# Kernel optimization log

Hardware: AMD Instinct MI355X
Metric: run time of the kernel (lower is better)

Reference implementation:

```python
import jax, jax.numpy as jnp
import numpy as np

VOCAB = 50000
EMB = 256
HID = 256
MAX_PRED = 30
B = 64
S_ENC = 100


def setup_inputs() -> dict:
    key = jax.random.key(0)
    ks = jax.random.split(key, 16)
    s = 1.0 / np.sqrt(HID)
    return {
        "comment": jax.random.randint(ks[0], (B, 29), 0, VOCAB),
        "comment_input": jax.random.randint(ks[1], (B, 30), 0, VOCAB),
        "tok_output": jax.random.normal(ks[2], (B, S_ENC, HID), jnp.float32),
        "tok_enc_hc": jax.random.normal(ks[3], (1, B, HID), jnp.float32),
        "sbtao_output": jax.random.normal(ks[4], (B, S_ENC, HID), jnp.float32),
        "wemb": jax.random.normal(ks[5], (VOCAB, EMB), jnp.float32) * 0.02,
        "W_ih": jax.random.uniform(ks[6], (3 * HID, EMB), jnp.float32, -s, s),
        "W_hh": jax.random.uniform(ks[7], (3 * HID, HID), jnp.float32, -s, s),
        "b_ih": jax.random.uniform(ks[8], (3 * HID,), jnp.float32, -s, s),
        "b_hh": jax.random.uniform(ks[9], (3 * HID,), jnp.float32, -s, s),
        "W1": jax.random.uniform(ks[10], (HID, 3 * HID), jnp.float32, -s, s),
        "b1": jax.random.uniform(ks[11], (HID,), jnp.float32, -s, s),
        "W2": jax.random.uniform(ks[12], (VOCAB, HID), jnp.float32, -s, s),
        "b2": jax.random.uniform(ks[13], (VOCAB,), jnp.float32, -s, s),
    }


def _decode(comment_input, T, tok_output, h0, sbtao_output,
            wemb, W_ih, W_hh, b_ih, b_hh, W1, b1, W2, b2):
    # h0: [B,H]. The torch code re-uses hidden=tok_enc_hc at EVERY step,
    # so each step is an independent GRU-cell step -> vectorize over T.
    bsz = comment_input.shape[0]
    H = h0.shape[-1]
    emb = wemb[comment_input[:, :T]]                      # [B,T,E]
    gi = emb @ W_ih.T + b_ih                              # [B,T,3H]
    gh = h0 @ W_hh.T + b_hh                               # [B,3H]
    gh = gh[:, None, :]                                   # broadcast over T
    r = jax.nn.sigmoid(gi[..., :H] + gh[..., :H])
    z = jax.nn.sigmoid(gi[..., H:2 * H] + gh[..., H:2 * H])
    n = jnp.tanh(gi[..., 2 * H:] + r * gh[..., 2 * H:])
    dec = (1.0 - z) * n + z * h0[:, None, :]              # [B,T,H]

    def attend(enc):  # enc: [B,S,H]
        S = enc.shape[1]
        # Faithful to torch: keys come from a RESHAPE [B,S,H] -> [B,H,S]
        # (memory reinterpretation), not a transpose.
        keys = enc.reshape(bsz, H, S)
        a = jax.nn.softmax(jnp.einsum('bth,bhs->bts', dec, keys), axis=-1)
        return jnp.einsum('bts,bsh->bth', a, enc)         # [B,T,H]

    ctx = attend(tok_output)
    ast_ctx = attend(sbtao_output)
    cat = jnp.concatenate([ctx, dec, ast_ctx], axis=-1)   # [B,T,3H]
    out = jax.nn.relu(cat @ W1.T + b1)                    # [B,T,H]
    out = jax.nn.relu(out @ W2.T + b2)                    # [B,T,V]
    logprobs = jax.nn.log_softmax(out, axis=-1)           # [B,T,V]
    return logprobs


def reference(comment, comment_input, tok_output, tok_enc_hc, sbtao_output,
              wemb, W_ih, W_hh, b_ih, b_hh, W1, b1, W2, b2):
    T = min(comment.shape[1] + 1, MAX_PRED)
    h0 = tok_enc_hc[0]
    logprobs = _decode(comment_input, T, tok_output, h0, sbtao_output,
                       wemb, W_ih, W_hh, b_ih, b_hh, W1, b1, W2, b2)
    seq = jnp.argmax(logprobs, axis=-1).astype(jnp.int64 if jax.config.jax_enable_x64 else jnp.int32)
    return seq, logprobs
```

## Files before the change

kernel.cpp:

```cpp
#include <hip/hip_runtime.h>
#include <hip/hip_bf16.h>
#include <math.h>

#define NROW 1920
#define VOCAB_ 50000
#define NPAD 50048
#define NBLK 391
#define LDBF 72

typedef __attribute__((ext_vector_type(8))) short short8;
typedef __attribute__((ext_vector_type(4))) float floatx4;

__device__ inline ushort f32_to_bf16_bits(float f) {
    union { float f; unsigned u; } v; v.f = f;
    unsigned u = v.u;
    u += 0x7fffu + ((u >> 16) & 1u);
    return (ushort)(u >> 16);
}

__global__ void gather_emb_kernel(const int* __restrict__ tokens,
                                  const float* __restrict__ wemb,
                                  float* __restrict__ emb) {
    int n = blockIdx.x;
    int e = threadIdx.x;
    int tok = tokens[n];
    emb[(size_t)n * 256 + e] = wemb[(size_t)tok * 256 + e];
}

template <bool RELU>
__global__ __launch_bounds__(256) void gemm_nt_kernel(
    const float* __restrict__ A, const float* __restrict__ Bm,
    const float* __restrict__ bias, float* __restrict__ C,
    int M, int N, int K) {
    __shared__ float As[32][68];
    __shared__ float Bs[32][68];

    const int tid = threadIdx.x;
    const int m0 = blockIdx.y * 64;
    const int n0 = blockIdx.x * 64;
    const int tx = tid & 15;
    const int ty = tid >> 4;
    const int lrow = tid >> 3;
    const int lcol = (tid & 7) * 4;

    float acc[4][4];
#pragma unroll
    for (int i = 0; i < 4; ++i)
#pragma unroll
        for (int j = 0; j < 4; ++j) acc[i][j] = 0.f;

    for (int k0 = 0; k0 < K; k0 += 32) {
#pragma unroll
        for (int half = 0; half < 2; ++half) {
            int m = lrow + half * 32;
            float4 av = *reinterpret_cast<const float4*>(
                A + (size_t)(m0 + m) * K + k0 + lcol);
            As[lcol + 0][m] = av.x; As[lcol + 1][m] = av.y;
            As[lcol + 2][m] = av.z; As[lcol + 3][m] = av.w;
            int n = lrow + half * 32;
            float4 bv = make_float4(0.f, 0.f, 0.f, 0.f);
            if (n0 + n < N)
                bv = *reinterpret_cast<const float4*>(
                    Bm + (size_t)(n0 + n) * K + k0 + lcol);
            Bs[lcol + 0][n] = bv.x; Bs[lcol + 1][n] = bv.y;
            Bs[lcol + 2][n] = bv.z; Bs[lcol + 3][n] = bv.w;
        }
        __syncthreads();
#pragma unroll
        for (int k = 0; k < 32; ++k) {
            float4 a4 = *reinterpret_cast<const float4*>(&As[k][ty * 4]);
            float4 b4 = *reinterpret_cast<const float4*>(&Bs[k][tx * 4]);
            float a[4] = {a4.x, a4.y, a4.z, a4.w};
            float b[4] = {b4.x, b4.y, b4.z, b4.w};
#pragma unroll
            for (int i = 0; i < 4; ++i)
#pragma unroll
                for (int j = 0; j < 4; ++j) acc[i][j] = fmaf(a[i], b[j], acc[i][j]);
        }
        __syncthreads();
    }
#pragma unroll
    for (int i = 0; i < 4; ++i) {
        int m = m0 + ty * 4 + i;
#pragma unroll
        for (int j = 0; j < 4; ++j) {
            int n = n0 + tx * 4 + j;
            if (n < N) {
                float v = acc[i][j] + bias[n];
                if (RELU) v = fmaxf(v, 0.f);
                C[(size_t)m * N + n] = v;
            }
        }
    }
}

__global__ void dec_kernel(const float* __restrict__ gi,
                           const float* __restrict__ gh,
                           const float* __restrict__ h0,
                           float* __restrict__ cat) {
    int n = blockIdx.x;
    int h = threadIdx.x;
    int b = n / 30;
    float gir = gi[(size_t)n * 768 + h];
    float giz = gi[(size_t)n * 768 + 256 + h];
    float gin = gi[(size_t)n * 768 + 512 + h];
    float ghr = gh[(size_t)b * 768 + h];
    float ghz = gh[(size_t)b * 768 + 256 + h];
    float ghn = gh[(size_t)b * 768 + 512 + h];
    float r = 1.f / (1.f + expf(-(gir + ghr)));
    float z = 1.f / (1.f + expf(-(giz + ghz)));
    float nn = tanhf(gin + r * ghn);
    float h0v = h0[(size_t)b * 256 + h];
    cat[(size_t)n * 768 + 256 + h] = (1.f - z) * nn + z * h0v;
}

__global__ __launch_bounds__(256) void attn_kernel(
    const float* __restrict__ enc, float* __restrict__ cat, int colbase) {
    __shared__ float decs[256];
    __shared__ float sc[100];
    __shared__ float red[2];

    int n = blockIdx.x;
    int b = n / 30;
    int tid = threadIdx.x;

    decs[tid] = cat[(size_t)n * 768 + 256 + tid];
    __syncthreads();
    const float* e = enc + (size_t)b * 25600;
    if (tid < 100) {
        float acc = 0.f;
        for (int h = 0; h < 256; ++h) acc = fmaf(decs[h], e[h * 100 + tid], acc);
        sc[tid] = acc;
    }
    __syncthreads();
    if (tid == 0) {
        float mx = sc[0];
        for (int s = 1; s < 100; ++s) mx = fmaxf(mx, sc[s]);
        red[0] = mx;
    }
    __syncthreads();
    if (tid < 100) sc[tid] = expf(sc[tid] - red[0]);
    __syncthreads();
    if (tid == 0) {
        float sum = 0.f;
        for (int s = 0; s < 100; ++s) sum += sc[s];
        red[1] = 1.f / sum;
    }
    __syncthreads();
    float inv = red[1];
    float acc = 0.f;
    for (int s = 0; s < 100; ++s) acc = fmaf(sc[s], e[s * 256 + tid], acc);
    cat[(size_t)n * 768 + colbase + tid] = acc * inv;
}

__global__ void conv_out1_kernel(const float* __restrict__ src, ushort* __restrict__ dst) {
    size_t i = (size_t)blockIdx.x * 256 + threadIdx.x;
    dst[i] = f32_to_bf16_bits(src[i]);
}

__global__ void conv_w2_kernel(const float* __restrict__ W2, ushort* __restrict__ Wb) {
    int row = blockIdx.x;
    int col = threadIdx.x;
    float v = (row < VOCAB_) ? W2[(size_t)row * 256 + col] : 0.f;
    Wb[(size_t)row * 256 + col] = f32_to_bf16_bits(v);
}

__global__ __launch_bounds__(256) void mfma_gemm_kernel(
    const ushort* __restrict__ Abf, const ushort* __restrict__ Bbf,
    const float* __restrict__ b2, float* __restrict__ C,
    float* __restrict__ pmax, float* __restrict__ psum) {
    __shared__ ushort As[128 * LDBF];
    __shared__ ushort Bs[128 * LDBF];
    __shared__ float pmL[128][2];
    __shared__ float psL[128][2];

    const int tid = threadIdx.x;
    const int m0 = blockIdx.x * 128;
    const int n0 = blockIdx.y * 128;
    const int nblk = blockIdx.y;
    const int wave = tid >> 6, lane = tid & 63;
    const int wm = wave >> 1, wn = wave & 1;
    const int q = lane >> 4, ln = lane & 15;

    const int srow = tid >> 1;
    const int sseg = (tid & 1) * 32;

    floatx4 acc[4][4];
#pragma unroll
    for (int i = 0; i < 4; ++i)
#pragma unroll
        for (int j = 0; j < 4; ++j) acc[i][j] = (floatx4)0.f;

    for (int k0 = 0; k0 < 256; k0 += 64) {
        const uint4* asrc = reinterpret_cast<const uint4*>(
            Abf + (size_t)(m0 + srow) * 256 + k0 + sseg);
        uint4 a0 = asrc[0], a1 = asrc[1], a2 = asrc[2], a3 = asrc[3];
        const uint4* bsrc = reinterpret_cast<const uint4*>(
            Bbf + (size_t)(n0 + srow) * 256 + k0 + sseg);
        uint4 c0 = bsrc[0], c1 = bsrc[1], c2 = bsrc[2], c3 = bsrc[3];
        __syncthreads();
        uint4* ad = reinterpret_cast<uint4*>(&As[srow * LDBF + sseg]);
        ad[0] = a0; ad[1] = a1; ad[2] = a2; ad[3] = a3;
        uint4* bd = reinterpret_cast<uint4*>(&Bs[srow * LDBF + sseg]);
        bd[0] = c0; bd[1] = c1; bd[2] = c2; bd[3] = c3;
        __syncthreads();
#pragma unroll
        for (int ks = 0; ks < 2; ++ks) {
            short8 af[4], bf[4];
#pragma unroll
            for (int mt = 0; mt < 4; ++mt)
                af[mt] = *reinterpret_cast<const short8*>(
                    &As[(wm * 64 + mt * 16 + ln) * LDBF + ks * 32 + q * 8]);
#pragma unroll
            for (int nt = 0; nt < 4; ++nt)
                bf[nt] = *reinterpret_cast<const short8*>(
                    &Bs[(wn * 64 + nt * 16 + ln) * LDBF + ks * 32 + q * 8]);
#pragma unroll
            for (int mt = 0; mt < 4; ++mt)
#pragma unroll
                for (int nt = 0; nt < 4; ++nt)
                    acc[mt][nt] = __builtin_amdgcn_mfma_f32_16x16x32_bf16(
                        af[mt], bf[nt], acc[mt][nt], 0, 0, 0);
        }
    }

    float bias[4]; int nn[4];
#pragma unroll
    for (int nt = 0; nt < 4; ++nt) {
        int n = n0 + wn * 64 + nt * 16 + ln;
        nn[nt] = n;
        bias[nt] = (n < VOCAB_) ? b2[n] : 0.f;
    }
#pragma unroll
    for (int mt = 0; mt < 4; ++mt) {
#pragma unroll
        for (int r = 0; r < 4; ++r) {
            int m = m0 + wm * 64 + mt * 16 + q * 4 + r;
            float vv[4]; float lmax = -1e30f;
#pragma unroll
            for (int nt = 0; nt < 4; ++nt) {
                float v = acc[mt][nt][r] + bias[nt];
                v = fmaxf(v, 0.f);
                if (nn[nt] < VOCAB_) C[(size_t)m * VOCAB_ + nn[nt]] = v;
                else v = -1e30f;
                vv[nt] = v;
                lmax = fmaxf(lmax, v);
            }
#pragma unroll
            for (int off = 1; off < 16; off <<= 1)
                lmax = fmaxf(lmax, __shfl_xor(lmax, off, 64));
            float ls = 0.f;
#pragma unroll
            for (int nt = 0; nt < 4; ++nt) ls += __expf(vv[nt] - lmax);
#pragma unroll
            for (int off = 1; off < 16; off <<= 1)
                ls += __shfl_xor(ls, off, 64);
            if (ln == 0) {
                int rl = wm * 64 + mt * 16 + q * 4 + r;
                pmL[rl][wn] = lmax;
                psL[rl][wn] = ls;
            }
        }
    }
    __syncthreads();
    if (tid < 128) {
        float m1 = pmL[tid][0], m2 = pmL[tid][1];
        float nm = fmaxf(m1, m2);
        float s = psL[tid][0] * __expf(m1 - nm) + psL[tid][1] * __expf(m2 - nm);
        pmax[(size_t)(m0 + tid) * NBLK + nblk] = nm;
        psum[(size_t)(m0 + tid) * NBLK + nblk] = s;
    }
}

__global__ __launch_bounds__(128) void reduce_rows_kernel(
    const float* __restrict__ pmax, const float* __restrict__ psum,
    float* __restrict__ row_max, float* __restrict__ row_lse) {
    __shared__ float sm[128], ss[128];
    int row = blockIdx.x, tid = threadIdx.x;
    const float* pm = pmax + (size_t)row * NBLK;
    const float* ps = psum + (size_t)row * NBLK;
    float m = -1e30f, s = 0.f;
    for (int i = tid; i < NBLK; i += 128) {
        float m2 = pm[i], s2 = ps[i];
        float nm = fmaxf(m, m2);
        s = s * __expf(m - nm) + s2 * __expf(m2 - nm);
        m = nm;
    }
    sm[tid] = m; ss[tid] = s;
    __syncthreads();
    for (int off = 64; off > 0; off >>= 1) {
        if (tid < off) {
            float m2 = sm[tid + off], s2 = ss[tid + off];
            float nm = fmaxf(sm[tid], m2);
            ss[tid] = ss[tid] * __expf(sm[tid] - nm) + s2 * __expf(m2 - nm);
            sm[tid] = nm;
        }
        __syncthreads();
    }
    if (tid == 0) {
        row_max[row] = sm[0];
        row_lse[row] = sm[0] + logf(ss[0]);
    }
}

__global__ __launch_bounds__(256) void final_kernel(
    float* __restrict__ logits, const float* __restrict__ row_max,
    const float* __restrict__ row_lse, const float* __restrict__ out1,
    const float* __restrict__ W2, const float* __restrict__ b2,
    float* __restrict__ seq) {
    __shared__ float o1s[256];
    __shared__ int cnt;
    __shared__ int cand[128];
    __shared__ double red[256];
    __shared__ double bestv_s;
    __shared__ int besti_s;

    int row = blockIdx.x, tid = threadIdx.x;
    if (tid == 0) { cnt = 0; bestv_s = -1e300; besti_s = 0x7fffffff; }
    o1s[tid] = out1[(size_t)row * 256 + tid];
    __syncthreads();

    float rmax = row_max[row], rlse = row_lse[row];
    float thr = rmax - 0.03f;
    float* p = logits + (size_t)row * VOCAB_;
    float4* p4 = reinterpret_cast<float4*>(p);
    for (int i = tid; i < VOCAB_ / 4; i += 256) {
        float4 v = p4[i];
        if (v.x >= thr) { int k = atomicAdd(&cnt, 1); if (k < 128) cand[k] = i * 4; }
        if (v.y >= thr) { int k = atomicAdd(&cnt, 1); if (k < 128) cand[k] = i * 4 + 1; }
        if (v.z >= thr) { int k = atomicAdd(&cnt, 1); if (k < 128) cand[k] = i * 4 + 2; }
        if (v.w >= thr) { int k = atomicAdd(&cnt, 1); if (k < 128) cand[k] = i * 4 + 3; }
        v.x -= rlse; v.y -= rlse; v.z -= rlse; v.w -= rlse;
        p4[i] = v;
    }
    __syncthreads();
    int nc = min(cnt, 128);
    for (int j = 0; j < nc; ++j) {
        int c = cand[j];
        red[tid] = (double)o1s[tid] * (double)W2[(size_t)c * 256 + tid];
        __syncthreads();
        for (int off = 128; off > 0; off >>= 1) {
            if (tid < off) red[tid] += red[tid + off];
            __syncthreads();
        }
        if (tid == 0) {
            double v = red[0] + (double)b2[c];
            if (v < 0.0) v = 0.0;
            if (v > bestv_s || (v == bestv_s && c < besti_s)) { bestv_s = v; besti_s = c; }
        }
        __syncthreads();
    }
    if (tid == 0) seq[row] = (float)besti_s;
}

extern "C" void kernel_launch(void* const* d_in, const int* in_sizes, int n_in,
                              void* d_out, int out_size, void* d_ws, size_t ws_size,
                              hipStream_t stream) {
    const int* comment_input = (const int*)d_in[1];
    const float* tok_output  = (const float*)d_in[2];
    const float* h0          = (const float*)d_in[3];
    const float* sbtao       = (const float*)d_in[4];
    const float* wemb        = (const float*)d_in[5];
    const float* W_ih        = (const float*)d_in[6];
    const float* W_hh        = (const float*)d_in[7];
    const float* b_ih        = (const float*)d_in[8];
    const float* b_hh        = (const float*)d_in[9];
    const float* W1          = (const float*)d_in[10];
    const float* b1          = (const float*)d_in[11];
    const float* W2          = (const float*)d_in[12];
    const float* b2          = (const float*)d_in[13];

    float* out    = (float*)d_out;
    float* seq    = out;
    float* logits = out + NROW;

    float* ws      = (float*)d_ws;
    float* emb     = ws;
    float* gi      = emb + 491520;
    float* gh      = gi + 1474560;
    float* cat     = gh + 49152;
    float* out1    = cat + 1474560;
    float* pmax    = out1 + 491520;
    float* psum    = pmax + 750720;
    float* row_max = psum + 750720;
    float* row_lse = row_max + 1920;
    ushort* out1b  = (ushort*)(row_lse + 1920);
    ushort* W2b    = (ushort*)(row_lse + 1920 + 245760);

    gather_emb_kernel<<<NROW, 256, 0, stream>>>(comment_input, wemb, emb);

    gemm_nt_kernel<false><<<dim3(12, 1), 256, 0, stream>>>(
        h0, W_hh, b_hh, gh, 64, 768, 256);
    gemm_nt_kernel<false><<<dim3(12, 30), 256, 0, stream>>>(
        emb, W_ih, b_ih, gi, NROW, 768, 256);
    dec_kernel<<<NROW, 256, 0, stream>>>(gi, gh, h0, cat);
    attn_kernel<<<NROW, 256, 0, stream>>>(tok_output, cat, 0);
    attn_kernel<<<NROW, 256, 0, stream>>>(sbtao, cat, 512);
    gemm_nt_kernel<true><<<dim3(4, 30), 256, 0, stream>>>(
        cat, W1, b1, out1, NROW, 256, 768);

    conv_out1_kernel<<<NROW, 256, 0, stream>>>(out1, out1b);
    conv_w2_kernel<<<NPAD, 256, 0, stream>>>(W2, W2b);

    mfma_gemm_kernel<<<dim3(15, NBLK), 256, 0, stream>>>(
        out1b, W2b, b2, logits, pmax, psum);

    reduce_rows_kernel<<<NROW, 128, 0, stream>>>(pmax, psum, row_max, row_lse);

    final_kernel<<<NROW, 256, 0, stream>>>(
        logits, row_max, row_lse, out1, W2, b2, seq);
}
```

Baseline: 972.3 us.

## Recompute logits GEMM in a second pass instead of rereading logits

```diff
diff --git a/kernel.cpp b/kernel.cpp
--- a/kernel.cpp
+++ b/kernel.cpp
@@ -7,6 +7,7 @@
 #define NPAD 50048
 #define NBLK 391
 #define LDBF 72
+#define CAP 128
 
 typedef __attribute__((ext_vector_type(8))) short short8;
 typedef __attribute__((ext_vector_type(4))) float floatx4;
@@ -165,10 +166,13 @@
     Wb[(size_t)row * 256 + col] = f32_to_bf16_bits(v);
 }
 
+template <int MODE>
 __global__ __launch_bounds__(256) void mfma_gemm_kernel(
     const ushort* __restrict__ Abf, const ushort* __restrict__ Bbf,
     const float* __restrict__ b2, float* __restrict__ C,
-    float* __restrict__ pmax, float* __restrict__ psum) {
+    float* __restrict__ pmax, float* __restrict__ psum,
+    const float* __restrict__ row_max, const float* __restrict__ row_lse,
+    int* __restrict__ cnt, int* __restrict__ cand) {
     __shared__ ushort As[128 * LDBF];
     __shared__ ushort Bs[128 * LDBF];
     __shared__ float pmL[128][2];
@@ -231,52 +235,77 @@
         nn[nt] = n;
         bias[nt] = (n < VOCAB_) ? b2[n] : 0.f;
     }
-#pragma unroll
-    for (int mt = 0; mt < 4; ++mt) {
-#pragma unroll
-        for (int r = 0; r < 4; ++r) {
-            int m = m0 + wm * 64 + mt * 16 + q * 4 + r;
-            float vv[4]; float lmax = -1e30f;
-#pragma unroll
-            for (int nt = 0; nt < 4; ++nt) {
-                float v = acc[mt][nt][r] + bias[nt];
-                v = fmaxf(v, 0.f);
-                if (nn[nt] < VOCAB_) C[(size_t)m * VOCAB_ + nn[nt]] = v;
-                else v = -1e30f;
-                vv[nt] = v;
-                lmax = fmaxf(lmax, v);
+
+    if (MODE == 0) {
+#pragma unroll
+        for (int mt = 0; mt < 4; ++mt) {
+#pragma unroll
+            for (int r = 0; r < 4; ++r) {
+                float vv[4]; float lmax = -1e30f;
+#pragma unroll
+                for (int nt = 0; nt < 4; ++nt) {
+                    float v = acc[mt][nt][r] + bias[nt];
+                    v = fmaxf(v, 0.f);
+                    if (nn[nt] >= VOCAB_) v = -1e30f;
+                    vv[nt] = v;
+                    lmax = fmaxf(lmax, v);
+                }
+#pragma unroll
+                for (int off = 1; off < 16; off <<= 1)
+                    lmax = fmaxf(lmax, __shfl_xor(lmax, off, 64));
+                float ls = 0.f;
+#pragma unroll
+                for (int nt = 0; nt < 4; ++nt) ls += __expf(vv[nt] - lmax);
+#pragma unroll
+                for (int off = 1; off < 16; off <<= 1)
+                    ls += __shfl_xor(ls, off, 64);
+                if (ln == 0) {
+                    int rl = wm * 64 + mt * 16 + q * 4 + r;
+                    pmL[rl][wn] = lmax;
+                    psL[rl][wn] = ls;
+                }
             }
-#pragma unroll
-            for (int off = 1; off < 16; off <<= 1)
-                lmax = fmaxf(lmax, __shfl_xor(lmax, off, 64));
-            float ls = 0.f;
-#pragma unroll
-            for (int nt = 0; nt < 4; ++nt) ls += __expf(vv[nt] - lmax);
-#pragma unroll
-            for (int off = 1; off < 16; off <<= 1)
-                ls += __shfl_xor(ls, off, 64);
-            if (ln == 0) {
-                int rl = wm * 64 + mt * 16 + q * 4 + r;
-                pmL[rl][wn] = lmax;
-                psL[rl][wn] = ls;
+        }
+        __syncthreads();
+        if (tid < 128) {
+            float m1 = pmL[tid][0], m2 = pmL[tid][1];
+            float nm = fmaxf(m1, m2);
+            float s = psL[tid][0] * __expf(m1 - nm) + psL[tid][1] * __expf(m2 - nm);
+            pmax[(size_t)(m0 + tid) * NBLK + nblk] = nm;
+            psum[(size_t)(m0 + tid) * NBLK + nblk] = s;
+        }
+    } else {
+#pragma unroll
+        for (int mt = 0; mt < 4; ++mt) {
+#pragma unroll
+            for (int r = 0; r < 4; ++r) {
+                int m = m0 + wm * 64 + mt * 16 + q * 4 + r;
+                float thr = row_max[m] - 0.03f;
+                float rl = row_lse[m];
+#pragma unroll
+                for (int nt = 0; nt < 4; ++nt) {
+                    if (nn[nt] < VOCAB_) {
+                        float v = acc[mt][nt][r] + bias[nt];
+                        v = fmaxf(v, 0.f);
+                        C[(size_t)m * VOCAB_ + nn[nt]] = v - rl;
+                        if (v >= thr) {
+                            int k = atomicAdd(&cnt[m], 1);
+                            if (k < CAP) cand[m * CAP + k] = nn[nt];
+                        }
+                    }
+                }
             }
         }
-    }
-    __syncthreads();
-    if (tid < 128) {
-        float m1 = pmL[tid][0], m2 = pmL[tid][1];
-        float nm = fmaxf(m1, m2);
-        float s = psL[tid][0] * __expf(m1 - nm) + psL[tid][1] * __expf(m2 - nm);
-        pmax[(size_t)(m0 + tid) * NBLK + nblk] = nm;
-        psum[(size_t)(m0 + tid) * NBLK + nblk] = s;
     }
 }
 
 __global__ __launch_bounds__(128) void reduce_rows_kernel(
     const float* __restrict__ pmax, const float* __restrict__ psum,
-    float* __restrict__ row_max, float* __restrict__ row_lse) {
+    float* __restrict__ row_max, float* __restrict__ row_lse,
+    int* __restrict__ cnt) {
     __shared__ float sm[128], ss[128];
     int row = blockIdx.x, tid = threadIdx.x;
+    if (tid == 0) cnt[row] = 0;
     const float* pm = pmax + (size_t)row * NBLK;
     const float* ps = psum + (size_t)row * NBLK;
     float m = -1e30f, s = 0.f;
@@ -303,40 +332,23 @@
     }
 }
 
-__global__ __launch_bounds__(256) void final_kernel(
-    float* __restrict__ logits, const float* __restrict__ row_max,
-    const float* __restrict__ row_lse, const float* __restrict__ out1,
-    const float* __restrict__ W2, const float* __restrict__ b2,
-    float* __restrict__ seq) {
+__global__ __launch_bounds__(256) void final_cand_kernel(
+    const int* __restrict__ cnt, const int* __restrict__ cand,
+    const float* __restrict__ out1, const float* __restrict__ W2,
+    const float* __restrict__ b2, float* __restrict__ seq) {
     __shared__ float o1s[256];
-    __shared__ int cnt;
-    __shared__ int cand[128];
     __shared__ double red[256];
     __shared__ double bestv_s;
     __shared__ int besti_s;
 
     int row = blockIdx.x, tid = threadIdx.x;
-    if (tid == 0) { cnt = 0; bestv_s = -1e300; besti_s = 0x7fffffff; }
+    if (tid == 0) { bestv_s = -1e300; besti_s = 0x7fffffff; }
     o1s[tid] = out1[(size_t)row * 256 + tid];
     __syncthreads();
 
-    float rmax = row_max[row], rlse = row_lse[row];
-    float thr = rmax - 0.03f;
-    float* p = logits + (size_t)row * VOCAB_;
-    float4* p4 = reinterpret_cast<float4*>(p);
-    for (int i = tid; i < VOCAB_ / 4; i += 256) {
-        float4 v = p4[i];
-        if (v.x >= thr) { int k = atomicAdd(&cnt, 1); if (k < 128) cand[k] = i * 4; }
-        if (v.y >= thr) { int k = atomicAdd(&cnt, 1); if (k < 128) cand[k] = i * 4 + 1; }
-        if (v.z >= thr) { int k = atomicAdd(&cnt, 1); if (k < 128) cand[k] = i * 4 + 2; }
-        if (v.w >= thr) { int k = atomicAdd(&cnt, 1); if (k < 128) cand[k] = i * 4 + 3; }
-        v.x -= rlse; v.y -= rlse; v.z -= rlse; v.w -= rlse;
-        p4[i] = v;
-    }
-    __syncthreads();
-    int nc = min(cnt, 128);
+    int nc = min(cnt[row], CAP);
     for (int j = 0; j < nc; ++j) {
-        int c = cand[j];
+        int c = cand[row * CAP + j];
         red[tid] = (double)o1s[tid] * (double)W2[(size_t)c * 256 + tid];
         __syncthreads();
         for (int off = 128; off > 0; off >>= 1) {
@@ -350,7 +362,7 @@
         }
         __syncthreads();
     }
-    if (tid == 0) seq[row] = (float)besti_s;
+    if (tid == 0) seq[row] = (float)(besti_s == 0x7fffffff ? 0 : besti_s);
 }
 
 extern "C" void kernel_launch(void* const* d_in, const int* in_sizes, int n_in,
@@ -386,6 +398,8 @@
     float* row_lse = row_max + 1920;
     ushort* out1b  = (ushort*)(row_lse + 1920);
     ushort* W2b    = (ushort*)(row_lse + 1920 + 245760);
+    int* cnt       = (int*)emb;
+    int* cand      = cnt + 1920;
 
     gather_emb_kernel<<<NROW, 256, 0, stream>>>(comment_input, wemb, emb);
 
@@ -402,11 +416,14 @@
     conv_out1_kernel<<<NROW, 256, 0, stream>>>(out1, out1b);
     conv_w2_kernel<<<NPAD, 256, 0, stream>>>(W2, W2b);
 
-    mfma_gemm_kernel<<<dim3(15, NBLK), 256, 0, stream>>>(
-        out1b, W2b, b2, logits, pmax, psum);
-
-    reduce_rows_kernel<<<NROW, 128, 0, stream>>>(pmax, psum, row_max, row_lse);
-
-    final_kernel<<<NROW, 256, 0, stream>>>(
-        logits, row_max, row_lse, out1, W2, b2, seq);
-}
+    mfma_gemm_kernel<0><<<dim3(15, NBLK), 256, 0, stream>>>(
+        out1b, W2b, b2, logits, pmax, psum, nullptr, nullptr, nullptr, nullptr);
+
+    reduce_rows_kernel<<<NROW, 128, 0, stream>>>(pmax, psum, row_max, row_lse, cnt);
+
+    mfma_gemm_kernel<1><<<dim3(15, NBLK), 256, 0, stream>>>(
+        out1b, W2b, b2, logits, nullptr, nullptr, row_max, row_lse, cnt, cand);
+
+    final_cand_kernel<<<NROW, 256, 0, stream>>>(
+        cnt, cand, out1, W2, b2, seq);
+}
```

Result: faster. 867.4 us (-10.8%).
